# Kernel optimization log

Hardware: AMD Instinct MI355X
Metric: run time of the kernel (lower is better)

## Reference

```python
import jax, jax.numpy as jnp
import numpy as np
from math import sqrt


def setup_inputs() -> dict:
    key = jax.random.key(0)
    k1, k2, k3 = jax.random.split(key, 3)
    B, L, H, E = 2, 2048, 16, 64
    queries = jax.random.normal(k1, (B, L, H, E), dtype=jnp.float32)
    keys = jax.random.normal(k2, (B, L, H, E), dtype=jnp.float32)
    values = jax.random.normal(k3, (B, L, H, E), dtype=jnp.float32)
    return {"queries": queries, "keys": keys, "values": values}


def reference(queries, keys, values):
    # queries: [B,L,H,E], keys: [B,S,H,E], values: [B,S,H,D]
    B, L, H, E = queries.shape
    S = keys.shape[1]
    scale = 1.0 / sqrt(E)
    # raw scores [B,H,L,S]
    scores = jnp.einsum('blhe,bshe->bhls', queries, keys)
    # triangular causal mask (True above diagonal -> masked)
    causal = jnp.triu(jnp.ones((L, S), dtype=bool), k=1)  # [L,S]
    scores = jnp.where(causal[None, None, :, :], -jnp.inf, scores)
    A = jax.nn.softmax(scale * scores, axis=-1)  # dropout p=0 -> identity
    V = jnp.einsum('bhls,bshd->blhd', A, values)
    return V
```

## Files before the change

kernel.cpp:

```cpp
#include <hip/hip_runtime.h>

typedef __attribute__((ext_vector_type(2))) __fp16 fp16x2;
typedef __attribute__((ext_vector_type(4))) _Float16 half4;
typedef __attribute__((ext_vector_type(8))) _Float16 half8;
typedef __attribute__((ext_vector_type(4))) float floatx4;

typedef union { half8 h8; half4 h4[2]; } h8split;

#define B_SZ  2
#define L_SEQ 2048
#define NH    16
#define EDIM  64
#define LOG2E 1.4426950408889634f
#define QSCALE (0.125f * LOG2E)

__device__ __forceinline__ int swz(int s, int ch) {
    return ch ^ (((s & 7) + 2 * (s >> 4)) & 7);
}

__global__ __launch_bounds__(256, 1)
void convert_kv(const float* __restrict__ K, const float* __restrict__ V,
                _Float16* __restrict__ Kh, _Float16* __restrict__ Vt)
{
    __shared__ __align__(16) _Float16 Tile[64 * 64];
    const int st = blockIdx.x & 31;
    const int h  = (blockIdx.x >> 5) & 15;
    const int b  = blockIdx.x >> 9;
    const int s0 = st * 64;
    const int t  = threadIdx.x;
    const int r  = t >> 2, c = t & 3;
    const size_t bh   = (size_t)b * NH + h;
    const size_t src  = (((size_t)b * L_SEQ + s0 + r) * NH + h) * EDIM + c * 16;
    const size_t cbase = bh * (size_t)(L_SEQ * EDIM) + (size_t)st * 4096;

    {
        const float4* kp = (const float4*)(K + src);
        float4 f[4];
#pragma unroll
        for (int i = 0; i < 4; ++i) f[i] = kp[i];
        _Float16 tmp[16];
#pragma unroll
        for (int i = 0; i < 4; ++i) {
            fp16x2 a  = __builtin_amdgcn_cvt_pkrtz(f[i].x, f[i].y);
            fp16x2 b2 = __builtin_amdgcn_cvt_pkrtz(f[i].z, f[i].w);
            tmp[4*i+0] = (_Float16)a[0];  tmp[4*i+1] = (_Float16)a[1];
            tmp[4*i+2] = (_Float16)b2[0]; tmp[4*i+3] = (_Float16)b2[1];
        }
        _Float16* kd = Kh + cbase + (size_t)(r >> 4) * 1024 + (c >> 1) * 512 + (r & 15) * 8;
        *(half8*)(kd + (((2 * c)     & 3) * 128)) = *(half8*)&tmp[0];
        *(half8*)(kd + (((2 * c + 1) & 3) * 128)) = *(half8*)&tmp[8];
    }
    {
        const float4* vp = (const float4*)(V + src);
        float4 f[4];
#pragma unroll
        for (int i = 0; i < 4; ++i) f[i] = vp[i];
        _Float16 tmp[16];
#pragma unroll
        for (int i = 0; i < 4; ++i) {
            fp16x2 a  = __builtin_amdgcn_cvt_pkrtz(f[i].x, f[i].y);
            fp16x2 b2 = __builtin_amdgcn_cvt_pkrtz(f[i].z, f[i].w);
            tmp[4*i+0] = (_Float16)a[0];  tmp[4*i+1] = (_Float16)a[1];
            tmp[4*i+2] = (_Float16)b2[0]; tmp[4*i+3] = (_Float16)b2[1];
        }
        _Float16* base = &Tile[r * 64];
        *(half8*)(base + swz(r, 2 * c)     * 8) = *(half8*)&tmp[0];
        *(half8*)(base + swz(r, 2 * c + 1) * 8) = *(half8*)&tmp[8];
    }
    __syncthreads();
    {
        const int d = t >> 2, seg = t & 3;
        _Float16 tmp[16];
#pragma unroll
        for (int i = 0; i < 16; ++i) {
            const int s = seg * 16 + i;
            tmp[i] = Tile[s * 64 + swz(s, d >> 3) * 8 + (d & 7)];
        }
        _Float16* vd = Vt + cbase + (size_t)seg * 1024 + (d >> 5) * 512
                       + (d & 15) * 8 + ((d >> 4) & 1) * 4;
#pragma unroll
        for (int kg = 0; kg < 4; ++kg)
            *(half4*)(vd + kg * 128) = *(half4*)&tmp[kg * 4];
    }
}

__global__ __launch_bounds__(256, 4)
void fa_fwd(const float* __restrict__ Q, const _Float16* __restrict__ Kh,
            const _Float16* __restrict__ Vt, float* __restrict__ O)
{
    __shared__ __align__(16) _Float16 Kb[2][4096];
    __shared__ __align__(16) _Float16 Vb[2][4096];

    const int i  = blockIdx.x;
    const int bh = i & 31;
    const int v  = i >> 5;
    const int u  = v & 7, j = v >> 3;
    const int tile = (j == 0) ? (31 - u) : (j == 1) ? u : (j == 2) ? (23 - u) : (8 + u);
    const int b    = bh >> 4;
    const int h    = bh & 15;
    const int wid  = threadIdx.x >> 6;
    const int lane = threadIdx.x & 63;
    const int ln16 = lane & 15;
    const int quad = lane >> 4;
    const int qrow0 = tile * 64;
    const int nch   = tile + 1;
    const int t16   = threadIdx.x * 16;
    const int lane8 = lane * 8;

    half8 qfA, qfB;
    {
        const float4* qp = (const float4*)(Q + (((size_t)b * L_SEQ + qrow0 + wid * 16 + ln16) * NH + h) * EDIM + quad * 8);
        float4 f0 = qp[0], f1 = qp[1];
        float4 f2 = qp[8], f3 = qp[9];
        fp16x2 t0 = __builtin_amdgcn_cvt_pkrtz(f0.x * QSCALE, f0.y * QSCALE);
        fp16x2 t1 = __builtin_amdgcn_cvt_pkrtz(f0.z * QSCALE, f0.w * QSCALE);
        fp16x2 t2 = __builtin_amdgcn_cvt_pkrtz(f1.x * QSCALE, f1.y * QSCALE);
        fp16x2 t3 = __builtin_amdgcn_cvt_pkrtz(f1.z * QSCALE, f1.w * QSCALE);
        qfA[0] = (_Float16)t0[0]; qfA[1] = (_Float16)t0[1];
        qfA[2] = (_Float16)t1[0]; qfA[3] = (_Float16)t1[1];
        qfA[4] = (_Float16)t2[0]; qfA[5] = (_Float16)t2[1];
        qfA[6] = (_Float16)t3[0]; qfA[7] = (_Float16)t3[1];
        t0 = __builtin_amdgcn_cvt_pkrtz(f2.x * QSCALE, f2.y * QSCALE);
        t1 = __builtin_amdgcn_cvt_pkrtz(f2.z * QSCALE, f2.w * QSCALE);
        t2 = __builtin_amdgcn_cvt_pkrtz(f3.x * QSCALE, f3.y * QSCALE);
        t3 = __builtin_amdgcn_cvt_pkrtz(f3.z * QSCALE, f3.w * QSCALE);
        qfB[0] = (_Float16)t0[0]; qfB[1] = (_Float16)t0[1];
        qfB[2] = (_Float16)t1[0]; qfB[3] = (_Float16)t1[1];
        qfB[4] = (_Float16)t2[0]; qfB[5] = (_Float16)t2[1];
        qfB[6] = (_Float16)t3[0]; qfB[7] = (_Float16)t3[1];
    }

    const char* kgb = (const char*)(Kh + (size_t)bh * (L_SEQ * EDIM));
    const char* vgb = (const char*)(Vt + (size_t)bh * (L_SEQ * EDIM));

    {
        half8 ka = *(const half8*)(kgb + t16);
        half8 kc = *(const half8*)(kgb + 4096 + t16);
        half8 va = *(const half8*)(vgb + t16);
        half8 vc = *(const half8*)(vgb + 4096 + t16);
        *(half8*)((char*)Kb[0] + t16)        = ka;
        *(half8*)((char*)Kb[0] + 4096 + t16) = kc;
        *(half8*)((char*)Vb[0] + t16)        = va;
        *(half8*)((char*)Vb[0] + 4096 + t16) = vc;
    }
    __syncthreads();

    floatx4 acc[4];
#pragma unroll
    for (int dt = 0; dt < 4; ++dt) acc[dt] = (floatx4){0.f, 0.f, 0.f, 0.f};
    float lp = 0.f;

    for (int it = 0; it < nch; ++it) {
        const bool last = (it + 1 >= nch);
        half8 ka, kc2, va, vc2;
        if (!last) {
            const char* ks = kgb + (size_t)(it + 1) * 8192;
            const char* vs = vgb + (size_t)(it + 1) * 8192;
            ka  = *(const half8*)(ks + t16);
            kc2 = *(const half8*)(ks + 4096 + t16);
            va  = *(const half8*)(vs + t16);
            vc2 = *(const half8*)(vs + 4096 + t16);
        }

        const _Float16* kc = Kb[it & 1];
        const _Float16* vv = Vb[it & 1];
        const bool masked = (it == nch - 1);
#pragma unroll
        for (int s = 0; s < 4; ++s) {
            half8 k0 = *(const half8*)(kc + s * 1024 + lane8);
            half8 k1 = *(const half8*)(kc + s * 1024 + 512 + lane8);
            floatx4 z = (floatx4){0.f, 0.f, 0.f, 0.f};
            z = __builtin_amdgcn_mfma_f32_16x16x32_f16(k0, qfA, z, 0, 0, 0);
            floatx4 st = __builtin_amdgcn_mfma_f32_16x16x32_f16(k1, qfB, z, 0, 0, 0);

            float p[4];
#pragma unroll
            for (int r = 0; r < 4; ++r) {
                float e = __builtin_amdgcn_exp2f(st[r]);
                if (masked) {
                    const int key = it * 64 + s * 16 + quad * 4 + r;
                    e = (key <= qrow0 + wid * 16 + ln16) ? e : 0.0f;
                }
                p[r] = e;
            }
            lp += (p[0] + p[1]) + (p[2] + p[3]);
            fp16x2 lo = __builtin_amdgcn_cvt_pkrtz(p[0], p[1]);
            fp16x2 hi = __builtin_amdgcn_cvt_pkrtz(p[2], p[3]);
            half4 pf;
            pf[0] = (_Float16)lo[0]; pf[1] = (_Float16)lo[1];
            pf[2] = (_Float16)hi[0]; pf[3] = (_Float16)hi[1];

            h8split u01, u23;
            u01.h8 = *(const half8*)(vv + s * 1024 + lane8);
            u23.h8 = *(const half8*)(vv + s * 1024 + 512 + lane8);
            acc[0] = __builtin_amdgcn_mfma_f32_16x16x16f16(u01.h4[0], pf, acc[0], 0, 0, 0);
            acc[1] = __builtin_amdgcn_mfma_f32_16x16x16f16(u01.h4[1], pf, acc[1], 0, 0, 0);
            acc[2] = __builtin_amdgcn_mfma_f32_16x16x16f16(u23.h4[0], pf, acc[2], 0, 0, 0);
            acc[3] = __builtin_amdgcn_mfma_f32_16x16x16f16(u23.h4[1], pf, acc[3], 0, 0, 0);
        }

        if (!last) {
            char* kd = (char*)Kb[(it + 1) & 1];
            char* vd = (char*)Vb[(it + 1) & 1];
            *(half8*)(kd + t16)        = ka;
            *(half8*)(kd + 4096 + t16) = kc2;
            *(half8*)(vd + t16)        = va;
            *(half8*)(vd + 4096 + t16) = vc2;
            __syncthreads();
        }
    }

    lp += __shfl_xor(lp, 16);
    lp += __shfl_xor(lp, 32);
    const float inv = 1.0f / lp;
    float* op = O + (((size_t)b * L_SEQ + qrow0 + wid * 16 + ln16) * NH + h) * EDIM;
#pragma unroll
    for (int dt = 0; dt < 4; ++dt) {
        float4 ov = {acc[dt][0] * inv, acc[dt][1] * inv,
                     acc[dt][2] * inv, acc[dt][3] * inv};
        *(float4*)(op + dt * 16 + quad * 4) = ov;
    }
}

extern "C" void kernel_launch(void* const* d_in, const int* in_sizes, int n_in,
                              void* d_out, int out_size, void* d_ws, size_t ws_size,
                              hipStream_t stream) {
    const float* Q = (const float*)d_in[0];
    const float* K = (const float*)d_in[1];
    const float* V = (const float*)d_in[2];
    float* O = (float*)d_out;
    _Float16* Kh = (_Float16*)d_ws;
    _Float16* Vt = Kh + (size_t)B_SZ * NH * L_SEQ * EDIM;
    convert_kv<<<dim3(B_SZ * NH * (L_SEQ / 64)), dim3(256), 0, stream>>>(K, V, Kh, Vt);
    fa_fwd<<<dim3(32 * 32), dim3(256), 0, stream>>>(Q, Kh, Vt, O);
}
```

Before: 118.9 us.

## Use two waves per block with two 16-row query groups each to reuse K/V fragments

The attention kernel now runs 128 threads (2 waves) per block instead of 4, and each wave handles two 16-row query groups (rows offset by 32). Each K and V fragment loaded from shared memory feeds the MFMAs of both groups, halving LDS reads per unit of compute. Each thread now stages twice as many K/V vectors into shared memory. Register pressure rises from the doubled accumulators and Q fragments, and there are fewer waves per block to hide latency.

```diff
diff --git a/kernel.cpp b/kernel.cpp
--- a/kernel.cpp
+++ b/kernel.cpp
@@ -84,7 +84,7 @@
     }
 }
 
-__global__ __launch_bounds__(256, 4)
+__global__ __launch_bounds__(128, 2)
 void fa_fwd(const float* __restrict__ Q, const _Float16* __restrict__ Kh,
             const _Float16* __restrict__ Vt, float* __restrict__ O)
 {
@@ -107,59 +107,58 @@
     const int t16   = threadIdx.x * 16;
     const int lane8 = lane * 8;
 
-    half8 qfA, qfB;
-    {
-        const float4* qp = (const float4*)(Q + (((size_t)b * L_SEQ + qrow0 + wid * 16 + ln16) * NH + h) * EDIM + quad * 8);
+    half8 qfA[2], qfB[2];
+#pragma unroll
+    for (int g = 0; g < 2; ++g) {
+        const float4* qp = (const float4*)(Q + (((size_t)b * L_SEQ + qrow0 + wid * 16 + g * 32 + ln16) * NH + h) * EDIM + quad * 8);
         float4 f0 = qp[0], f1 = qp[1];
         float4 f2 = qp[8], f3 = qp[9];
         fp16x2 t0 = __builtin_amdgcn_cvt_pkrtz(f0.x * QSCALE, f0.y * QSCALE);
         fp16x2 t1 = __builtin_amdgcn_cvt_pkrtz(f0.z * QSCALE, f0.w * QSCALE);
         fp16x2 t2 = __builtin_amdgcn_cvt_pkrtz(f1.x * QSCALE, f1.y * QSCALE);
         fp16x2 t3 = __builtin_amdgcn_cvt_pkrtz(f1.z * QSCALE, f1.w * QSCALE);
-        qfA[0] = (_Float16)t0[0]; qfA[1] = (_Float16)t0[1];
-        qfA[2] = (_Float16)t1[0]; qfA[3] = (_Float16)t1[1];
-        qfA[4] = (_Float16)t2[0]; qfA[5] = (_Float16)t2[1];
-        qfA[6] = (_Float16)t3[0]; qfA[7] = (_Float16)t3[1];
+        qfA[g][0] = (_Float16)t0[0]; qfA[g][1] = (_Float16)t0[1];
+        qfA[g][2] = (_Float16)t1[0]; qfA[g][3] = (_Float16)t1[1];
+        qfA[g][4] = (_Float16)t2[0]; qfA[g][5] = (_Float16)t2[1];
+        qfA[g][6] = (_Float16)t3[0]; qfA[g][7] = (_Float16)t3[1];
         t0 = __builtin_amdgcn_cvt_pkrtz(f2.x * QSCALE, f2.y * QSCALE);
         t1 = __builtin_amdgcn_cvt_pkrtz(f2.z * QSCALE, f2.w * QSCALE);
         t2 = __builtin_amdgcn_cvt_pkrtz(f3.x * QSCALE, f3.y * QSCALE);
         t3 = __builtin_amdgcn_cvt_pkrtz(f3.z * QSCALE, f3.w * QSCALE);
-        qfB[0] = (_Float16)t0[0]; qfB[1] = (_Float16)t0[1];
-        qfB[2] = (_Float16)t1[0]; qfB[3] = (_Float16)t1[1];
-        qfB[4] = (_Float16)t2[0]; qfB[5] = (_Float16)t2[1];
-        qfB[6] = (_Float16)t3[0]; qfB[7] = (_Float16)t3[1];
+        qfB[g][0] = (_Float16)t0[0]; qfB[g][1] = (_Float16)t0[1];
+        qfB[g][2] = (_Float16)t1[0]; qfB[g][3] = (_Float16)t1[1];
+        qfB[g][4] = (_Float16)t2[0]; qfB[g][5] = (_Float16)t2[1];
+        qfB[g][6] = (_Float16)t3[0]; qfB[g][7] = (_Float16)t3[1];
     }
 
     const char* kgb = (const char*)(Kh + (size_t)bh * (L_SEQ * EDIM));
     const char* vgb = (const char*)(Vt + (size_t)bh * (L_SEQ * EDIM));
 
-    {
-        half8 ka = *(const half8*)(kgb + t16);
-        half8 kc = *(const half8*)(kgb + 4096 + t16);
-        half8 va = *(const half8*)(vgb + t16);
-        half8 vc = *(const half8*)(vgb + 4096 + t16);
-        *(half8*)((char*)Kb[0] + t16)        = ka;
-        *(half8*)((char*)Kb[0] + 4096 + t16) = kc;
-        *(half8*)((char*)Vb[0] + t16)        = va;
-        *(half8*)((char*)Vb[0] + 4096 + t16) = vc;
+#pragma unroll
+    for (int k = 0; k < 4; ++k) {
+        *(half8*)((char*)Kb[0] + t16 + k * 2048) = *(const half8*)(kgb + t16 + k * 2048);
+        *(half8*)((char*)Vb[0] + t16 + k * 2048) = *(const half8*)(vgb + t16 + k * 2048);
     }
     __syncthreads();
 
-    floatx4 acc[4];
-#pragma unroll
-    for (int dt = 0; dt < 4; ++dt) acc[dt] = (floatx4){0.f, 0.f, 0.f, 0.f};
-    float lp = 0.f;
+    floatx4 acc[4][2];
+#pragma unroll
+    for (int dt = 0; dt < 4; ++dt)
+#pragma unroll
+        for (int g = 0; g < 2; ++g) acc[dt][g] = (floatx4){0.f, 0.f, 0.f, 0.f};
+    float lp[2] = {0.f, 0.f};
 
     for (int it = 0; it < nch; ++it) {
         const bool last = (it + 1 >= nch);
-        half8 ka, kc2, va, vc2;
+        half8 stK[4], stV[4];
         if (!last) {
             const char* ks = kgb + (size_t)(it + 1) * 8192;
             const char* vs = vgb + (size_t)(it + 1) * 8192;
-            ka  = *(const half8*)(ks + t16);
-            kc2 = *(const half8*)(ks + 4096 + t16);
-            va  = *(const half8*)(vs + t16);
-            vc2 = *(const half8*)(vs + 4096 + t16);
+#pragma unroll
+            for (int k = 0; k < 4; ++k) {
+                stK[k] = *(const half8*)(ks + t16 + k * 2048);
+                stV[k] = *(const half8*)(vs + t16 + k * 2048);
+            }
         }
 
         const _Float16* kc = Kb[it & 1];
@@ -169,56 +168,65 @@
         for (int s = 0; s < 4; ++s) {
             half8 k0 = *(const half8*)(kc + s * 1024 + lane8);
             half8 k1 = *(const half8*)(kc + s * 1024 + 512 + lane8);
-            floatx4 z = (floatx4){0.f, 0.f, 0.f, 0.f};
-            z = __builtin_amdgcn_mfma_f32_16x16x32_f16(k0, qfA, z, 0, 0, 0);
-            floatx4 st = __builtin_amdgcn_mfma_f32_16x16x32_f16(k1, qfB, z, 0, 0, 0);
-
-            float p[4];
-#pragma unroll
-            for (int r = 0; r < 4; ++r) {
-                float e = __builtin_amdgcn_exp2f(st[r]);
-                if (masked) {
-                    const int key = it * 64 + s * 16 + quad * 4 + r;
-                    e = (key <= qrow0 + wid * 16 + ln16) ? e : 0.0f;
-                }
-                p[r] = e;
-            }
-            lp += (p[0] + p[1]) + (p[2] + p[3]);
-            fp16x2 lo = __builtin_amdgcn_cvt_pkrtz(p[0], p[1]);
-            fp16x2 hi = __builtin_amdgcn_cvt_pkrtz(p[2], p[3]);
-            half4 pf;
-            pf[0] = (_Float16)lo[0]; pf[1] = (_Float16)lo[1];
-            pf[2] = (_Float16)hi[0]; pf[3] = (_Float16)hi[1];
-
             h8split u01, u23;
             u01.h8 = *(const half8*)(vv + s * 1024 + lane8);
             u23.h8 = *(const half8*)(vv + s * 1024 + 512 + lane8);
-            acc[0] = __builtin_amdgcn_mfma_f32_16x16x16f16(u01.h4[0], pf, acc[0], 0, 0, 0);
-            acc[1] = __builtin_amdgcn_mfma_f32_16x16x16f16(u01.h4[1], pf, acc[1], 0, 0, 0);
-            acc[2] = __builtin_amdgcn_mfma_f32_16x16x16f16(u23.h4[0], pf, acc[2], 0, 0, 0);
-            acc[3] = __builtin_amdgcn_mfma_f32_16x16x16f16(u23.h4[1], pf, acc[3], 0, 0, 0);
+
+#pragma unroll
+            for (int g = 0; g < 2; ++g) {
+                floatx4 z = (floatx4){0.f, 0.f, 0.f, 0.f};
+                z = __builtin_amdgcn_mfma_f32_16x16x32_f16(k0, qfA[g], z, 0, 0, 0);
+                floatx4 st = __builtin_amdgcn_mfma_f32_16x16x32_f16(k1, qfB[g], z, 0, 0, 0);
+
+                float p[4];
+#pragma unroll
+                for (int r = 0; r < 4; ++r) {
+                    float e = __builtin_amdgcn_exp2f(st[r]);
+                    if (masked) {
+                        const int key = it * 64 + s * 16 + quad * 4 + r;
+                        e = (key <= qrow0 + wid * 16 + g * 32 + ln16) ? e : 0.0f;
+                    }
+                    p[r] = e;
+                }
+                lp[g] += (p[0] + p[1]) + (p[2] + p[3]);
+                fp16x2 lo = __builtin_amdgcn_cvt_pkrtz(p[0], p[1]);
+                fp16x2 hi = __builtin_amdgcn_cvt_pkrtz(p[2], p[3]);
+                half4 pf;
+                pf[0] = (_Float16)lo[0]; pf[1] = (_Float16)lo[1];
+                pf[2] = (_Float16)hi[0]; pf[3] = (_Float16)hi[1];
+
+                acc[0][g] = __builtin_amdgcn_mfma_f32_16x16x16f16(u01.h4[0], pf, acc[0][g], 0, 0, 0);
+                acc[1][g] = __builtin_amdgcn_mfma_f32_16x16x16f16(u01.h4[1], pf, acc[1][g], 0, 0, 0);
+                acc[2][g] = __builtin_amdgcn_mfma_f32_16x16x16f16(u23.h4[0], pf, acc[2][g], 0, 0, 0);
+                acc[3][g] = __builtin_amdgcn_mfma_f32_16x16x16f16(u23.h4[1], pf, acc[3][g], 0, 0, 0);
+            }
         }
 
         if (!last) {
             char* kd = (char*)Kb[(it + 1) & 1];
             char* vd = (char*)Vb[(it + 1) & 1];
-            *(half8*)(kd + t16)        = ka;
-            *(half8*)(kd + 4096 + t16) = kc2;
-            *(half8*)(vd + t16)        = va;
-            *(half8*)(vd + 4096 + t16) = vc2;
+#pragma unroll
+            for (int k = 0; k < 4; ++k) {
+                *(half8*)(kd + t16 + k * 2048) = stK[k];
+                *(half8*)(vd + t16 + k * 2048) = stV[k];
+            }
             __syncthreads();
         }
     }
 
-    lp += __shfl_xor(lp, 16);
-    lp += __shfl_xor(lp, 32);
-    const float inv = 1.0f / lp;
-    float* op = O + (((size_t)b * L_SEQ + qrow0 + wid * 16 + ln16) * NH + h) * EDIM;
-#pragma unroll
-    for (int dt = 0; dt < 4; ++dt) {
-        float4 ov = {acc[dt][0] * inv, acc[dt][1] * inv,
-                     acc[dt][2] * inv, acc[dt][3] * inv};
-        *(float4*)(op + dt * 16 + quad * 4) = ov;
+#pragma unroll
+    for (int g = 0; g < 2; ++g) {
+        float l = lp[g];
+        l += __shfl_xor(l, 16);
+        l += __shfl_xor(l, 32);
+        const float inv = 1.0f / l;
+        float* op = O + (((size_t)b * L_SEQ + qrow0 + wid * 16 + g * 32 + ln16) * NH + h) * EDIM;
+#pragma unroll
+        for (int dt = 0; dt < 4; ++dt) {
+            float4 ov = {acc[dt][g][0] * inv, acc[dt][g][1] * inv,
+                         acc[dt][g][2] * inv, acc[dt][g][3] * inv};
+            *(float4*)(op + dt * 16 + quad * 4) = ov;
+        }
     }
 }
 
@@ -232,5 +240,5 @@
     _Float16* Kh = (_Float16*)d_ws;
     _Float16* Vt = Kh + (size_t)B_SZ * NH * L_SEQ * EDIM;
     convert_kv<<<dim3(B_SZ * NH * (L_SEQ / 64)), dim3(256), 0, stream>>>(K, V, Kh, Vt);
-    fa_fwd<<<dim3(32 * 32), dim3(256), 0, stream>>>(Q, Kh, Vt, O);
-}
+    fa_fwd<<<dim3(32 * 32), dim3(128), 0, stream>>>(Q, Kh, Vt, O);
+}
```

Measured after the change: 121.9 us. 1.02x slower.

## Use 16x16x32 MFMA for PV by pairing key subtiles and relaying out V

Applied to the files above, without the earlier changes.

Processes two 16-key subtiles at a time so the P·V product uses the K=32 MFMA instead of two K=16 MFMAs per output block. The V-transpose layout in the conversion kernel is changed so each lane's half8 holds the 8 keys matching the packed P fragment. This halves the number of PV MFMA issues and interleaves two QK score computations, but raises register pressure per iteration.

```diff
diff --git a/kernel.cpp b/kernel.cpp
--- a/kernel.cpp
+++ b/kernel.cpp
@@ -4,8 +4,6 @@
 typedef __attribute__((ext_vector_type(4))) _Float16 half4;
 typedef __attribute__((ext_vector_type(8))) _Float16 half8;
 typedef __attribute__((ext_vector_type(4))) float floatx4;
-
-typedef union { half8 h8; half4 h4[2]; } h8split;
 
 #define B_SZ  2
 #define L_SEQ 2048
@@ -76,8 +74,8 @@
             const int s = seg * 16 + i;
             tmp[i] = Tile[s * 64 + swz(s, d >> 3) * 8 + (d & 7)];
         }
-        _Float16* vd = Vt + cbase + (size_t)seg * 1024 + (d >> 5) * 512
-                       + (d & 15) * 8 + ((d >> 4) & 1) * 4;
+        _Float16* vd = Vt + cbase + (size_t)(seg >> 1) * 2048 + (d >> 4) * 512
+                       + (d & 15) * 8 + (seg & 1) * 4;
 #pragma unroll
         for (int kg = 0; kg < 4; ++kg)
             *(half4*)(vd + kg * 128) = *(half4*)&tmp[kg * 4];
@@ -166,37 +164,53 @@
         const _Float16* vv = Vb[it & 1];
         const bool masked = (it == nch - 1);
 #pragma unroll
-        for (int s = 0; s < 4; ++s) {
-            half8 k0 = *(const half8*)(kc + s * 1024 + lane8);
-            half8 k1 = *(const half8*)(kc + s * 1024 + 512 + lane8);
-            floatx4 z = (floatx4){0.f, 0.f, 0.f, 0.f};
-            z = __builtin_amdgcn_mfma_f32_16x16x32_f16(k0, qfA, z, 0, 0, 0);
-            floatx4 st = __builtin_amdgcn_mfma_f32_16x16x32_f16(k1, qfB, z, 0, 0, 0);
-
-            float p[4];
+        for (int sp = 0; sp < 2; ++sp) {
+            half8 k0a = *(const half8*)(kc + (2 * sp)     * 1024 + lane8);
+            half8 k1a = *(const half8*)(kc + (2 * sp)     * 1024 + 512 + lane8);
+            half8 k0b = *(const half8*)(kc + (2 * sp + 1) * 1024 + lane8);
+            half8 k1b = *(const half8*)(kc + (2 * sp + 1) * 1024 + 512 + lane8);
+            floatx4 za = (floatx4){0.f, 0.f, 0.f, 0.f};
+            za = __builtin_amdgcn_mfma_f32_16x16x32_f16(k0a, qfA, za, 0, 0, 0);
+            floatx4 sta = __builtin_amdgcn_mfma_f32_16x16x32_f16(k1a, qfB, za, 0, 0, 0);
+            floatx4 zb = (floatx4){0.f, 0.f, 0.f, 0.f};
+            zb = __builtin_amdgcn_mfma_f32_16x16x32_f16(k0b, qfA, zb, 0, 0, 0);
+            floatx4 stb = __builtin_amdgcn_mfma_f32_16x16x32_f16(k1b, qfB, zb, 0, 0, 0);
+
+            float pa[4], pb[4];
 #pragma unroll
             for (int r = 0; r < 4; ++r) {
-                float e = __builtin_amdgcn_exp2f(st[r]);
+                float ea = __builtin_amdgcn_exp2f(sta[r]);
+                float eb = __builtin_amdgcn_exp2f(stb[r]);
                 if (masked) {
-                    const int key = it * 64 + s * 16 + quad * 4 + r;
-                    e = (key <= qrow0 + wid * 16 + ln16) ? e : 0.0f;
+                    const int keya = it * 64 + (2 * sp)     * 16 + quad * 4 + r;
+                    const int keyb = it * 64 + (2 * sp + 1) * 16 + quad * 4 + r;
+                    const int qk = qrow0 + wid * 16 + ln16;
+                    ea = (keya <= qk) ? ea : 0.0f;
+                    eb = (keyb <= qk) ? eb : 0.0f;
                 }
-                p[r] = e;
+                pa[r] = ea;
+                pb[r] = eb;
             }
-            lp += (p[0] + p[1]) + (p[2] + p[3]);
-            fp16x2 lo = __builtin_amdgcn_cvt_pkrtz(p[0], p[1]);
-            fp16x2 hi = __builtin_amdgcn_cvt_pkrtz(p[2], p[3]);
-            half4 pf;
-            pf[0] = (_Float16)lo[0]; pf[1] = (_Float16)lo[1];
-            pf[2] = (_Float16)hi[0]; pf[3] = (_Float16)hi[1];
-
-            h8split u01, u23;
-            u01.h8 = *(const half8*)(vv + s * 1024 + lane8);
-            u23.h8 = *(const half8*)(vv + s * 1024 + 512 + lane8);
-            acc[0] = __builtin_amdgcn_mfma_f32_16x16x16f16(u01.h4[0], pf, acc[0], 0, 0, 0);
-            acc[1] = __builtin_amdgcn_mfma_f32_16x16x16f16(u01.h4[1], pf, acc[1], 0, 0, 0);
-            acc[2] = __builtin_amdgcn_mfma_f32_16x16x16f16(u23.h4[0], pf, acc[2], 0, 0, 0);
-            acc[3] = __builtin_amdgcn_mfma_f32_16x16x16f16(u23.h4[1], pf, acc[3], 0, 0, 0);
+            lp += (pa[0] + pa[1]) + (pa[2] + pa[3]);
+            lp += (pb[0] + pb[1]) + (pb[2] + pb[3]);
+            fp16x2 la = __builtin_amdgcn_cvt_pkrtz(pa[0], pa[1]);
+            fp16x2 ha = __builtin_amdgcn_cvt_pkrtz(pa[2], pa[3]);
+            fp16x2 lb = __builtin_amdgcn_cvt_pkrtz(pb[0], pb[1]);
+            fp16x2 hb = __builtin_amdgcn_cvt_pkrtz(pb[2], pb[3]);
+            half8 pf;
+            pf[0] = (_Float16)la[0]; pf[1] = (_Float16)la[1];
+            pf[2] = (_Float16)ha[0]; pf[3] = (_Float16)ha[1];
+            pf[4] = (_Float16)lb[0]; pf[5] = (_Float16)lb[1];
+            pf[6] = (_Float16)hb[0]; pf[7] = (_Float16)hb[1];
+
+            half8 v0 = *(const half8*)(vv + sp * 2048 +        lane8);
+            half8 v1 = *(const half8*)(vv + sp * 2048 +  512 + lane8);
+            half8 v2 = *(const half8*)(vv + sp * 2048 + 1024 + lane8);
+            half8 v3 = *(const half8*)(vv + sp * 2048 + 1536 + lane8);
+            acc[0] = __builtin_amdgcn_mfma_f32_16x16x32_f16(v0, pf, acc[0], 0, 0, 0);
+            acc[1] = __builtin_amdgcn_mfma_f32_16x16x32_f16(v1, pf, acc[1], 0, 0, 0);
+            acc[2] = __builtin_amdgcn_mfma_f32_16x16x32_f16(v2, pf, acc[2], 0, 0, 0);
+            acc[3] = __builtin_amdgcn_mfma_f32_16x16x32_f16(v3, pf, acc[3], 0, 0, 0);
         }
 
         if (!last) {
```

New measurement: 116.5 us. 1.02x faster.
